# Optimization experiments

Measured on AMD Instinct MI355X. Metric: run time of the kernel, lower is better.

Reference implementation:

```python
import jax, jax.numpy as jnp
import numpy as np

THETA = 1.0
V_TH = 1.0       # spikingjelly IFNode default v_threshold
SG_ALPHA = 4.0   # spikingjelly surrogate.Sigmoid default alpha


@jax.custom_vjp
def heaviside(x):
    # spike = 1 if membrane - threshold >= 0
    return (x >= 0).astype(x.dtype)

def _heaviside_fwd(x):
    return (x >= 0).astype(x.dtype), x

def _heaviside_bwd(x, g):
    s = jax.nn.sigmoid(SG_ALPHA * x)
    return (g * SG_ALPHA * s * (1.0 - s),)

heaviside.defvjp(_heaviside_fwd, _heaviside_bwd)


@jax.custom_vjp
def spike_aggregate(spike_out, z_total):
    return spike_out

def _sa_fwd(spike_out, z_total):
    return spike_out, z_total

def _sa_bwd(z_total, g):
    surrogate = (z_total > 0).astype(g.dtype) / THETA
    return (jnp.zeros_like(g), g * surrogate)

spike_aggregate.defvjp(_sa_fwd, _sa_bwd)


def setup_inputs() -> dict:
    key = jax.random.key(0)
    k_x, k_w1, k_b1, k_w2, k_b2 = jax.random.split(key, 5)
    B, D_in, H, D_out = 4096, 784, 800, 10
    x = jax.random.uniform(k_x, (B, D_in), dtype=jnp.float32)
    # nn.Linear-style init: U(-1/sqrt(fan_in), 1/sqrt(fan_in))
    s1 = 1.0 / np.sqrt(D_in)
    s2 = 1.0 / np.sqrt(H)
    W1 = jax.random.uniform(k_w1, (H, D_in), jnp.float32, -s1, s1)
    b1 = jax.random.uniform(k_b1, (H,), jnp.float32, -s1, s1)
    W2 = jax.random.uniform(k_w2, (D_out, H), jnp.float32, -s2, s2)
    b2 = jax.random.uniform(k_b2, (D_out,), jnp.float32, -s2, s2)
    return {"x": x, "W1": W1, "b1": b1, "W2": W2, "b2": b2, "T_sim": 32}


def reference(x, W1, b1, W2, b2, T_sim):
    B = x.shape[0]
    x = x.reshape(B, -1)
    # fixed Bernoulli rate encoding (rand_like(x) < x)
    u = jax.random.uniform(jax.random.key(42), x.shape, dtype=x.dtype)
    x_fixed = (u < x).astype(x.dtype)
    # fc1 input is the same every timestep -> compute once
    cur1 = x_fixed @ W1.T + b1                     # [B, 800]

    def step(carry, _):
        v1, v2, count, z_total = carry
        h1 = v1 + cur1
        spk1 = heaviside(h1 - V_TH)
        v1 = h1 * (1.0 - jax.lax.stop_gradient(spk1))  # hard reset to 0, detach_reset
        cur2 = spk1 @ W2.T + b2                    # [B, 10]
        z_total = z_total + cur2
        h2 = v2 + cur2
        spk2 = heaviside(h2 - V_TH)
        v2 = h2 * (1.0 - jax.lax.stop_gradient(spk2))
        count = count + spk2
        return (v1, v2, count, z_total), None

    H, D_out = W1.shape[0], W2.shape[0]
    init = (jnp.zeros((B, H), x.dtype), jnp.zeros((B, D_out), x.dtype),
            jnp.zeros((B, D_out), x.dtype), jnp.zeros((B, D_out), x.dtype))
    (v1, v2, count, z_total), _ = jax.lax.scan(step, init, None, length=T_sim)
    return spike_aggregate(count, z_total)
```

## Files before the change

### kernel.cpp

```cpp
#include <hip/hip_runtime.h>
#include <stdint.h>

#define B_ROWS 4096
#define D_IN   784
#define H_DIM  800
#define D_OUT  10
#define T_SIM  32
#define N_ELEM (B_ROWS * D_IN)
#define CAP    512

__device__ __forceinline__ void threefry2x32(uint32_t k0, uint32_t k1,
                                             uint32_t& x0, uint32_t& x1) {
  uint32_t ks0 = k0, ks1 = k1, ks2 = k0 ^ k1 ^ 0x1BD11BDAu;
  x0 += ks0; x1 += ks1;
#define TF_RND(r) { x0 += x1; x1 = (x1 << (r)) | (x1 >> (32 - (r))); x1 ^= x0; }
  TF_RND(13) TF_RND(15) TF_RND(26) TF_RND(6)
  x0 += ks1; x1 += ks2 + 1u;
  TF_RND(17) TF_RND(29) TF_RND(16) TF_RND(24)
  x0 += ks2; x1 += ks0 + 2u;
  TF_RND(13) TF_RND(15) TF_RND(26) TF_RND(6)
  x0 += ks0; x1 += ks1 + 3u;
  TF_RND(17) TF_RND(29) TF_RND(16) TF_RND(24)
  x0 += ks1; x1 += ks2 + 4u;
  TF_RND(13) TF_RND(15) TF_RND(26) TF_RND(6)
  x0 += ks2; x1 += ks0 + 5u;
#undef TF_RND
}

__global__ __launch_bounds__(256) void gen_xfixed(const float* __restrict__ x,
                                                  float* __restrict__ xf) {
  int i = blockIdx.x * blockDim.x + threadIdx.x;
  if (i >= N_ELEM) return;
  uint32_t c0 = 0u, c1 = (uint32_t)i;
  threefry2x32(0u, 42u, c0, c1);
  uint32_t bits = c0 ^ c1;
  float u = __uint_as_float((bits >> 9) | 0x3F800000u) - 1.0f;
  xf[i] = (u < x[i]) ? 1.0f : 0.0f;
}

#define BM 64
#define BN 64
#define BK 16

__global__ __launch_bounds__(256) void gemm_periods(const float* __restrict__ xf,
                                                    const float* __restrict__ W1,
                                                    const float* __restrict__ b1,
                                                    uint8_t* __restrict__ pb) {
  __shared__ __align__(16) float As[BK][BM + 4];
  __shared__ __align__(16) float Bs[BK][BN + 4];
  const int m0 = blockIdx.y * BM;
  const int n0 = blockIdx.x * BN;
  const int t  = threadIdx.x;
  const int tx = t & 15, ty = t >> 4;
  const int sM = t >> 2;
  const int sK = (t & 3) * 4;
  const int hB = n0 + sM;
  const bool bOK = (hB < H_DIM);
  const float* aptr = xf + (m0 + sM) * D_IN + sK;
  const float* bptr = W1 + (bOK ? hB : 0) * D_IN + sK;

  float4 a4 = *(const float4*)(aptr);
  float4 b4 = *(const float4*)(bptr);
  if (!bOK) { b4.x = b4.y = b4.z = b4.w = 0.0f; }

  float acc[4][4] = {};
  for (int kt = 0; kt < D_IN; kt += BK) {
    As[sK + 0][sM] = a4.x; As[sK + 1][sM] = a4.y;
    As[sK + 2][sM] = a4.z; As[sK + 3][sM] = a4.w;
    Bs[sK + 0][sM] = b4.x; Bs[sK + 1][sM] = b4.y;
    Bs[sK + 2][sM] = b4.z; Bs[sK + 3][sM] = b4.w;
    __syncthreads();
    if (kt + BK < D_IN) {
      a4 = *(const float4*)(aptr + kt + BK);
      b4 = *(const float4*)(bptr + kt + BK);
      if (!bOK) { b4.x = b4.y = b4.z = b4.w = 0.0f; }
    }
#pragma unroll
    for (int kk = 0; kk < BK; kk++) {
      float4 av = *(const float4*)&As[kk][ty * 4];
      float4 bv = *(const float4*)&Bs[kk][tx * 4];
      float a[4] = {av.x, av.y, av.z, av.w};
      float b[4] = {bv.x, bv.y, bv.z, bv.w};
#pragma unroll
      for (int mi = 0; mi < 4; mi++)
#pragma unroll
        for (int ni = 0; ni < 4; ni++)
          acc[mi][ni] = __builtin_fmaf(a[mi], b[ni], acc[mi][ni]);
    }
    __syncthreads();
  }
  const int hOut = n0 + tx * 4;
  if (hOut < H_DIM) {
    float4 bb = *(const float4*)&b1[hOut];
#pragma unroll
    for (int mi = 0; mi < 4; mi++) {
      int m = m0 + ty * 4 + mi;
      float c4[4] = {acc[mi][0] + bb.x, acc[mi][1] + bb.y,
                     acc[mi][2] + bb.z, acc[mi][3] + bb.w};
      uint32_t packed = 0;
#pragma unroll
      for (int ni = 0; ni < 4; ni++) {
        float c = c4[ni];
        float v = 0.0f;
        int p = 0;
#pragma unroll 1
        for (int s = 1; s <= T_SIM; s++) {
          float h1 = v + c;
          if (h1 >= 1.0f) { p = s; break; }
          v = h1;
        }
        packed |= (uint32_t)p << (8 * ni);
      }
      *(uint32_t*)&pb[(size_t)m * H_DIM + hOut] = packed;
    }
  }
}

__global__ __launch_bounds__(320) void snn_scan(const uint8_t* __restrict__ pb,
                                                const float* __restrict__ W2,
                                                const float* __restrict__ b2,
                                                float* __restrict__ out) {
  __shared__ __align__(16) float W2T[H_DIM * D_OUT];
  __shared__ __align__(8) uint2 pkS[2][CAP];
  __shared__ int      lenS[2];
  __shared__ uint32_t mtbl[T_SIM + 1];
  __shared__ float    c2s[2][T_SIM][D_OUT];
  __shared__ float    b2f[D_OUT];
  const int tid  = threadIdx.x;
  const int row0 = blockIdx.x * 2;

  if (tid <= T_SIM) {
    uint32_t mk = 0;
    if (tid) for (int s = tid; s <= T_SIM; s += tid) mk |= 1u << (s - 1);
    mtbl[tid] = mk;
  }
  if (tid < D_OUT) b2f[tid] = b2[tid];
  __syncthreads();

  if (tid < 128) {
    const int r = tid >> 6, ln = tid & 63;
    const uint64_t lm = (1ull << ln) - 1ull;
    const uint8_t* prow = pb + (size_t)(row0 + r) * H_DIM;
    uint8_t pv[13];
#pragma unroll
    for (int ch = 0; ch < 13; ++ch) {
      int h = ch * 64 + ln;
      pv[ch] = (h < H_DIM) ? prow[h] : (uint8_t)0;
    }
    int off = 0;
#pragma unroll
    for (int ch = 0; ch < 13; ++ch) {
      bool g = (pv[ch] != 0);
      uint64_t bal = __ballot(g);
      int pos = off + __popcll(bal & lm);
      if (g && pos < CAP) {
        uint2 pk;
        pk.x = (uint32_t)((ch * 64 + ln) * 40);
        pk.y = mtbl[pv[ch]];
        pkS[r][pos] = pk;
      }
      off += __popcll(bal);
    }
    if (ln == 0) lenS[r] = off;
  } else {
    for (int e = tid - 128; e < H_DIM * D_OUT; e += 192) {
      int o = e / H_DIM, h = e - o * H_DIM;
      W2T[h * D_OUT + o] = W2[e];
    }
  }
  __syncthreads();

  const int L0 = min(lenS[0], CAP), L1 = min(lenS[1], CAP);
  const bool ovf = (lenS[0] > CAP) || (lenS[1] > CAP);
  const int Lpad = (max(L0, L1) + 63) & ~63;

  for (int e = tid; e < 2 * CAP; e += 320) {
    int r = e >= CAP ? 1 : 0, i = e - r * CAP;
    if (i >= (r ? L1 : L0) && i < Lpad) { pkS[r][i].x = 0u; pkS[r][i].y = 0u; }
  }
  __syncthreads();

  {
    const int j = tid >> 6;
    const int lane = tid & 63;
    const int t = lane & 31;
    const int r = lane >> 5;
    float s0 = 0.0f, s1 = 0.0f;
    if (!ovf) {
      const uint2* pp = pkS[r];
      const char* wbase = (const char*)W2T + 8 * j;
#pragma unroll 4
      for (int i = 0; i < Lpad; ++i) {
        uint2 pk = pp[i];
        float2 w = *(const float2*)(wbase + pk.x);
        bool g = (pk.y >> t) & 1u;
        s0 += g ? w.x : 0.0f;
        s1 += g ? w.y : 0.0f;
      }
    } else {
      const uint8_t* prow = pb + (size_t)(row0 + r) * H_DIM;
      const uint32_t vbit = 1u << t;
      for (int h = 0; h < H_DIM; ++h) {
        uint32_t mk = mtbl[prow[h]];
        float2 w = *(const float2*)&W2T[h * D_OUT + 2 * j];
        s0 += (mk & vbit) ? w.x : 0.0f;
        s1 += (mk & vbit) ? w.y : 0.0f;
      }
    }
    c2s[r][t][2 * j]     = s0;
    c2s[r][t][2 * j + 1] = s1;
  }
  __syncthreads();

  if (tid < 2 * D_OUT) {
    const int r = tid / D_OUT, o = tid % D_OUT;
    const float bb = b2f[o];
    float v = 0.0f; int cnt = 0;
#pragma unroll
    for (int t = 0; t < T_SIM; ++t) {
      float cur2 = c2s[r][t][o] + bb;
      float h2 = v + cur2;
      bool spk = (h2 >= 1.0f);
      cnt += spk ? 1 : 0;
      v = spk ? 0.0f : h2;
    }
    out[(size_t)(row0 + r) * D_OUT + o] = (float)cnt;
  }
}

extern "C" void kernel_launch(void* const* d_in, const int* in_sizes, int n_in,
                              void* d_out, int out_size, void* d_ws, size_t ws_size,
                              hipStream_t stream) {
  const float* x  = (const float*)d_in[0];
  const float* W1 = (const float*)d_in[1];
  const float* b1 = (const float*)d_in[2];
  const float* W2 = (const float*)d_in[3];
  const float* b2 = (const float*)d_in[4];
  float* outp = (float*)d_out;

  float*   xf = (float*)d_ws;
  uint8_t* pbuf = (uint8_t*)(xf + N_ELEM);

  gen_xfixed<<<N_ELEM / 256, 256, 0, stream>>>(x, xf);

  dim3 g1((H_DIM + BN - 1) / BN, B_ROWS / BM);
  gemm_periods<<<g1, 256, 0, stream>>>(xf, W1, b1, pbuf);

  snn_scan<<<B_ROWS / 2, 320, 0, stream>>>(pbuf, W2, b2, outp);
}
```

Measured before the change: 286.4 us.

## Emit 32-bit spike masks from GEMM and slim the scan kernel's shared memory

The GEMM epilogue now writes a full 32-bit spike-time mask per neuron instead of a one-byte period, so the scan kernel no longer builds or looks up a mask table. The scan kernel also zero-pads its compaction lists inside the compaction warp, which removes one block-wide barrier. It reuses the packed-list buffer for the per-timestep currents and lowers the list capacity, cutting shared memory to allow more resident blocks. In exchange the mask buffer is four times larger in global memory traffic, and rows with more active neurons now hit the slow overflow path more often.

```diff
diff --git a/kernel.cpp b/kernel.cpp
--- a/kernel.cpp
+++ b/kernel.cpp
@@ -7,7 +7,7 @@
 #define D_OUT  10
 #define T_SIM  32
 #define N_ELEM (B_ROWS * D_IN)
-#define CAP    512
+#define CAP    448
 
 __device__ __forceinline__ void threefry2x32(uint32_t k0, uint32_t k1,
                                              uint32_t& x0, uint32_t& x1) {
@@ -42,10 +42,10 @@
 #define BN 64
 #define BK 16
 
-__global__ __launch_bounds__(256) void gemm_periods(const float* __restrict__ xf,
-                                                    const float* __restrict__ W1,
-                                                    const float* __restrict__ b1,
-                                                    uint8_t* __restrict__ pb) {
+__global__ __launch_bounds__(256) void gemm_masks(const float* __restrict__ xf,
+                                                  const float* __restrict__ W1,
+                                                  const float* __restrict__ b1,
+                                                  uint32_t* __restrict__ mb) {
   __shared__ __align__(16) float As[BK][BM + 4];
   __shared__ __align__(16) float Bs[BK][BN + 4];
   const int m0 = blockIdx.y * BM;
@@ -97,7 +97,7 @@
       int m = m0 + ty * 4 + mi;
       float c4[4] = {acc[mi][0] + bb.x, acc[mi][1] + bb.y,
                      acc[mi][2] + bb.z, acc[mi][3] + bb.w};
-      uint32_t packed = 0;
+      uint32_t mk4[4];
 #pragma unroll
       for (int ni = 0; ni < 4; ni++) {
         float c = c4[ni];
@@ -109,57 +109,56 @@
           if (h1 >= 1.0f) { p = s; break; }
           v = h1;
         }
-        packed |= (uint32_t)p << (8 * ni);
-      }
-      *(uint32_t*)&pb[(size_t)m * H_DIM + hOut] = packed;
-    }
-  }
-}
-
-__global__ __launch_bounds__(320) void snn_scan(const uint8_t* __restrict__ pb,
+        uint32_t mk = 0;
+        if (p) for (int s = p; s <= T_SIM; s += p) mk |= 1u << (s - 1);
+        mk4[ni] = mk;
+      }
+      *(uint4*)&mb[(size_t)m * H_DIM + hOut] =
+          make_uint4(mk4[0], mk4[1], mk4[2], mk4[3]);
+    }
+  }
+}
+
+__global__ __launch_bounds__(320) void snn_scan(const uint32_t* __restrict__ mb,
                                                 const float* __restrict__ W2,
                                                 const float* __restrict__ b2,
                                                 float* __restrict__ out) {
   __shared__ __align__(16) float W2T[H_DIM * D_OUT];
-  __shared__ __align__(8) uint2 pkS[2][CAP];
-  __shared__ int      lenS[2];
-  __shared__ uint32_t mtbl[T_SIM + 1];
-  __shared__ float    c2s[2][T_SIM][D_OUT];
-  __shared__ float    b2f[D_OUT];
+  __shared__ __align__(16) uint2 pkS[2][CAP];
+  __shared__ int   lenS[2];
+  __shared__ float b2f[D_OUT];
+  float* c2s = (float*)&pkS[0][0];
   const int tid  = threadIdx.x;
   const int row0 = blockIdx.x * 2;
 
-  if (tid <= T_SIM) {
-    uint32_t mk = 0;
-    if (tid) for (int s = tid; s <= T_SIM; s += tid) mk |= 1u << (s - 1);
-    mtbl[tid] = mk;
-  }
   if (tid < D_OUT) b2f[tid] = b2[tid];
-  __syncthreads();
 
   if (tid < 128) {
     const int r = tid >> 6, ln = tid & 63;
     const uint64_t lm = (1ull << ln) - 1ull;
-    const uint8_t* prow = pb + (size_t)(row0 + r) * H_DIM;
-    uint8_t pv[13];
+    const uint32_t* mrow = mb + (size_t)(row0 + r) * H_DIM;
+    uint32_t mv[13];
 #pragma unroll
     for (int ch = 0; ch < 13; ++ch) {
       int h = ch * 64 + ln;
-      pv[ch] = (h < H_DIM) ? prow[h] : (uint8_t)0;
+      mv[ch] = (h < H_DIM) ? mrow[h] : 0u;
     }
     int off = 0;
 #pragma unroll
     for (int ch = 0; ch < 13; ++ch) {
-      bool g = (pv[ch] != 0);
+      bool g = (mv[ch] != 0u);
       uint64_t bal = __ballot(g);
       int pos = off + __popcll(bal & lm);
       if (g && pos < CAP) {
-        uint2 pk;
-        pk.x = (uint32_t)((ch * 64 + ln) * 40);
-        pk.y = mtbl[pv[ch]];
+        uint2 pk; pk.x = (uint32_t)((ch * 64 + ln) * 40); pk.y = mv[ch];
         pkS[r][pos] = pk;
       }
       off += __popcll(bal);
+    }
+    if (off <= CAP) {
+      int lp = (off + 63) & ~63;
+      int i = off + ln;
+      if (i < lp) { pkS[r][i].x = 0u; pkS[r][i].y = 0u; }
     }
     if (ln == 0) lenS[r] = off;
   } else {
@@ -170,23 +169,15 @@
   }
   __syncthreads();
 
-  const int L0 = min(lenS[0], CAP), L1 = min(lenS[1], CAP);
+  float s0 = 0.0f, s1 = 0.0f;
+  const int j = tid >> 6;
+  const int lane = tid & 63;
+  const int t = lane & 31;
+  const int r = lane >> 5;
   const bool ovf = (lenS[0] > CAP) || (lenS[1] > CAP);
-  const int Lpad = (max(L0, L1) + 63) & ~63;
-
-  for (int e = tid; e < 2 * CAP; e += 320) {
-    int r = e >= CAP ? 1 : 0, i = e - r * CAP;
-    if (i >= (r ? L1 : L0) && i < Lpad) { pkS[r][i].x = 0u; pkS[r][i].y = 0u; }
-  }
-  __syncthreads();
-
   {
-    const int j = tid >> 6;
-    const int lane = tid & 63;
-    const int t = lane & 31;
-    const int r = lane >> 5;
-    float s0 = 0.0f, s1 = 0.0f;
     if (!ovf) {
+      const int Lpad = (lenS[r] + 63) & ~63;
       const uint2* pp = pkS[r];
       const char* wbase = (const char*)W2T + 8 * j;
 #pragma unroll 4
@@ -198,33 +189,34 @@
         s1 += g ? w.y : 0.0f;
       }
     } else {
-      const uint8_t* prow = pb + (size_t)(row0 + r) * H_DIM;
+      const uint32_t* mrow = mb + (size_t)(row0 + r) * H_DIM;
       const uint32_t vbit = 1u << t;
       for (int h = 0; h < H_DIM; ++h) {
-        uint32_t mk = mtbl[prow[h]];
+        uint32_t mk = mrow[h];
         float2 w = *(const float2*)&W2T[h * D_OUT + 2 * j];
         s0 += (mk & vbit) ? w.x : 0.0f;
         s1 += (mk & vbit) ? w.y : 0.0f;
       }
     }
-    c2s[r][t][2 * j]     = s0;
-    c2s[r][t][2 * j + 1] = s1;
   }
   __syncthreads();
+  c2s[((r * T_SIM) + t) * D_OUT + 2 * j]     = s0;
+  c2s[((r * T_SIM) + t) * D_OUT + 2 * j + 1] = s1;
+  __syncthreads();
 
   if (tid < 2 * D_OUT) {
-    const int r = tid / D_OUT, o = tid % D_OUT;
+    const int rr = tid / D_OUT, o = tid % D_OUT;
     const float bb = b2f[o];
     float v = 0.0f; int cnt = 0;
 #pragma unroll
-    for (int t = 0; t < T_SIM; ++t) {
-      float cur2 = c2s[r][t][o] + bb;
+    for (int tt = 0; tt < T_SIM; ++tt) {
+      float cur2 = c2s[((rr * T_SIM) + tt) * D_OUT + o] + bb;
       float h2 = v + cur2;
       bool spk = (h2 >= 1.0f);
       cnt += spk ? 1 : 0;
       v = spk ? 0.0f : h2;
     }
-    out[(size_t)(row0 + r) * D_OUT + o] = (float)cnt;
+    out[(size_t)(row0 + rr) * D_OUT + o] = (float)cnt;
   }
 }
 
@@ -238,13 +230,13 @@
   const float* b2 = (const float*)d_in[4];
   float* outp = (float*)d_out;
 
-  float*   xf = (float*)d_ws;
-  uint8_t* pbuf = (uint8_t*)(xf + N_ELEM);
+  float*    xf = (float*)d_ws;
+  uint32_t* mbuf = (uint32_t*)(xf + N_ELEM);
 
   gen_xfixed<<<N_ELEM / 256, 256, 0, stream>>>(x, xf);
 
   dim3 g1((H_DIM + BN - 1) / BN, B_ROWS / BM);
-  gemm_periods<<<g1, 256, 0, stream>>>(xf, W1, b1, pbuf);
-
-  snn_scan<<<B_ROWS / 2, 320, 0, stream>>>(pbuf, W2, b2, outp);
-}
+  gemm_masks<<<g1, 256, 0, stream>>>(xf, W1, b1, mbuf);
+
+  snn_scan<<<B_ROWS / 2, 320, 0, stream>>>(mbuf, W2, b2, outp);
+}
```

After: 280.8 us. No clear change (-1.9%).
